# Performance work log

Measured on AMD Instinct MI355X. Metric: run time of the kernel, lower is better.

Reference implementation:

```python
import jax, jax.numpy as jnp
import numpy as np

B, T, CIN, H, W = 256, 19, 3, 24, 24
HID, LAST, K = 64, 128, 512
CC = 0.25  # commitment cost
NUM_DEC_LAYERS = 19


def setup_inputs() -> dict:
    key = jax.random.key(0)
    ks = jax.random.split(key, 19)
    def rn(k, shape, scale=0.05):
        return jax.random.normal(k, shape, jnp.float32) * scale
    return dict(
        x=jax.random.normal(ks[0], (B, T, CIN, H, W), jnp.float32),
        eps=jax.random.normal(ks[1], (B, LAST), jnp.float32),
        emb=jax.random.normal(ks[2], (K, HID), jnp.float32),
        enc_w0=rn(ks[3], (HID, CIN, 3, 3)), enc_w0_b=rn(ks[4], (HID,)),
        enc_w1=rn(ks[5], (2 * LAST, HID, 8, 8)), enc_w1_b=rn(ks[6], (2 * LAST,)),
        enc_r0=rn(ks[7], (HID, HID)), enc_r0_b=rn(ks[8], (HID,)),
        enc_lin_w=rn(ks[9], (2 * LAST, 2 * LAST)), enc_lin_b=rn(ks[10], (2 * LAST,)),
        dec_w0=rn(ks[11], (HID, CIN, 3, 3)), dec_w0_b=rn(ks[12], (CIN,)),
        dec_w1=rn(ks[13], (LAST, HID, 8, 8)), dec_w1_b=rn(ks[14], (HID,)),
        dec_r0=rn(ks[15], (HID, HID)), dec_r0_b=rn(ks[16], (HID,)),
        dec_lin_w=rn(ks[17], (LAST, LAST)), dec_lin_b=rn(ks[18], (LAST,)),
    )


def reference(x, eps, emb, enc_w0, enc_w0_b, enc_w1, enc_w1_b, enc_r0, enc_r0_b,
              enc_lin_w, enc_lin_b, dec_w0, dec_w0_b, dec_w1, dec_w1_b,
              dec_r0, dec_r0_b, dec_lin_w, dec_lin_b):
    relu = jax.nn.relu

    # ---- encoder (conv-RNN over time) ----
    def conv0(xt):  # Conv2d(CIN->HID, k=3, s=3): 24x24 -> 8x8
        y = jax.lax.conv_general_dilated(
            xt, enc_w0, (3, 3), 'VALID',
            dimension_numbers=('NCHW', 'OIHW', 'NCHW'))
        return y + enc_w0_b[None, :, None, None]

    def contract(h1):  # Conv2d(HID->2*LAST, k=8) on 8x8 == full contraction
        return jnp.einsum('bchw,ochw->bo', h1, enc_w1) + enc_w1_b

    h1 = relu(conv0(x[:, 0]))
    h2 = relu(contract(h1))

    def enc_step(carry, xt):
        h1, h2 = carry
        h1 = relu(conv0(xt) + jnp.einsum('bchw,oc->bohw', h1, enc_r0)
                  + enc_r0_b[None, :, None, None])
        h2h = relu(contract(h1))
        h2 = relu(h2h + h2 @ enc_lin_w.T + enc_lin_b)
        return (h1, h2), None

    (h1, h2), _ = jax.lax.scan(enc_step, (h1, h2), jnp.swapaxes(x[:, 1:], 0, 1))

    # ---- VQ (EMA codebook lookup; codebook carries no grad) ----
    zin = jnp.transpose(h1, (0, 2, 3, 1))        # [B, 8, 8, HID]
    flat = zin.reshape(-1, HID)                   # [B*64, HID]
    d = (jnp.sum(flat * flat, 1, keepdims=True)
         + jnp.sum(emb * emb, 1) - 2.0 * flat @ emb.T)
    idx = jnp.argmin(d, 1)                        # [B*64]
    q = emb[idx].reshape(zin.shape)
    loss_vq = CC * jnp.mean((jax.lax.stop_gradient(q) - zin) ** 2)
    q_st = zin + jax.lax.stop_gradient(q - zin)   # straight-through
    quantized = jnp.transpose(q_st, (0, 3, 1, 2)) # [B, HID, 8, 8]
    counts = jnp.zeros((K,), flat.dtype).at[idx].add(1.0)
    avg = counts / flat.shape[0]
    perplexity = jnp.exp(-jnp.sum(avg * jnp.log(avg + 1e-10)))

    # ---- KL(q(z|x) || N(0,1)) and reparam sample ----
    mu, logvar = jnp.split(h2, 2, axis=1)
    kl = jnp.mean(jnp.sum(0.5 * (jnp.exp(logvar) + mu * mu - 1.0 - logvar), axis=1))
    h2s = mu + jnp.exp(0.5 * logvar) * eps

    # ---- decoder (conv-RNN emitting 19 frames) ----
    def dec_update(h1c, h2c):
        h2c = relu(h2c @ dec_lin_w.T + dec_lin_b)
        h1h = jnp.einsum('bchw,oc->bohw', h1c, dec_r0) + dec_r0_b[None, :, None, None]
        h1l = jnp.einsum('bc,cohw->bohw', h2c, dec_w1) + dec_w1_b[None, :, None, None]
        return relu(h1h + h1l), h2c

    h1d, h2d = dec_update(quantized, h2s)  # i == 0: no emitted frame

    def dec_step(carry, _):
        h1c, h2c = carry
        h1c, h2c = dec_update(h1c, h2c)
        # ConvTranspose2d(HID->CIN, k=3, s=3): non-overlapping -> einsum + reshape
        y = jnp.einsum('bchw,coij->bohiwj', h1c, dec_w0).reshape(
            h1c.shape[0], CIN, 24, 24)
        layer = jax.nn.elu(y + dec_w0_b[None, :, None, None])
        return (h1c, h2c), layer

    _, layers = jax.lax.scan(dec_step, (h1d, h2d), None, length=NUM_DEC_LAYERS)
    x_tilde = jnp.swapaxes(layers, 0, 1)  # [B, 19, CIN, 24, 24]

    return (loss_vq, kl, x_tilde, perplexity)
```

## Files before the change

### kernel.cpp

```cpp
#include <hip/hip_runtime.h>
#include <math.h>

#define RL(x) __builtin_amdgcn_readfirstlane(x)

typedef short  s16x8 __attribute__((ext_vector_type(8)));
typedef float  f32x4 __attribute__((ext_vector_type(4)));

__device__ __forceinline__ float relu_(float v) { return v > 0.f ? v : 0.f; }
__device__ __forceinline__ unsigned short f2bf(float f) {
  unsigned u = __float_as_uint(f);
  u += 0x7FFFu + ((u >> 16) & 1u);
  return (unsigned short)(u >> 16);
}
__device__ __forceinline__ float bf2f(unsigned short h) {
  return __uint_as_float((unsigned)h << 16);
}

__global__ __launch_bounds__(256) void k_prep(
    const float* __restrict__ w1, const float* __restrict__ linw,
    const float* __restrict__ dlinw, const float* __restrict__ emb,
    const float* __restrict__ dw1,
    unsigned short* __restrict__ w1b, float* __restrict__ linT,
    float* __restrict__ dlinT, float* __restrict__ embsq,
    unsigned short* __restrict__ dw1b,
    float* __restrict__ scal, float* __restrict__ counts)
{
  int bid = blockIdx.x, tid = threadIdx.x;
  if (bid < 64) {
    #pragma unroll
    for (int j = 0; j < 32; ++j) {
      int idx = bid * 16384 + j * 512 + tid * 2;
      float2 v = *(const float2*)(w1 + idx);
      unsigned pk = ((unsigned)f2bf(v.y) << 16) | (unsigned)f2bf(v.x);
      *(unsigned*)&w1b[idx] = pk;
    }
    return;
  }
  if (bid == 84) {
    if (tid < 2) scal[tid] = 0.f;
    for (int j = tid; j < 512; j += 256) counts[j] = 0.f;
    return;
  }
  if (bid >= 85) {
    __shared__ float tbuf[64 * 65];
    int idx = bid - 85;
    int r0 = (idx >> 6) * 64, c0 = (idx & 63) * 64;
    int lane = tid & 63, grp = tid >> 6;
    for (int pp = 0; pp < 16; ++pp) {
      int rr = pp * 4 + grp;
      tbuf[rr * 65 + lane] = dw1[(size_t)(r0 + rr) * 4096 + c0 + lane];
    }
    __syncthreads();
    for (int pp = 0; pp < 16; ++pp) {
      int cc = pp * 4 + grp;
      dw1b[(size_t)(c0 + cc) * 128 + r0 + lane] = f2bf(tbuf[lane * 65 + cc]);
    }
    return;
  }
  if (bid >= 82) {
    int k = (bid - 82) * 256 + tid;
    const float* e = emb + k * 64;
    float s0 = 0, s1 = 0, s2 = 0, s3 = 0;
    #pragma unroll
    for (int c = 0; c < 64; c += 4) {
      s0 += e[c] * e[c]; s1 += e[c+1] * e[c+1];
      s2 += e[c+2] * e[c+2]; s3 += e[c+3] * e[c+3];
    }
    embsq[k] = (s0 + s1) + (s2 + s3);
    return;
  }
  __shared__ float buf[64 * 65];
  const float* in; float* out; int R, C, tr, tc;
  if (bid < 80) { in = linw;  out = linT;  R = 256; C = 256; tr = (bid - 64) >> 2; tc = (bid - 64) & 3; }
  else          { in = dlinw; out = dlinT; R = 128; C = 128; tr = (bid - 80) >> 1; tc = (bid - 80) & 1; }
  int r0 = tr * 64, c0 = tc * 64;
  int lane = tid & 63, grp = tid >> 6;
  for (int pp = 0; pp < 16; ++pp) {
    int rr = pp * 4 + grp;
    buf[rr * 65 + lane] = in[(r0 + rr) * C + c0 + lane];
  }
  __syncthreads();
  for (int pp = 0; pp < 16; ++pp) {
    int cc = pp * 4 + grp;
    out[(c0 + cc) * R + r0 + lane] = buf[lane * 65 + cc];
  }
}

__global__ __launch_bounds__(256) void k_conv0(
    const float* __restrict__ x, const float* __restrict__ w0,
    float* __restrict__ xconv)
{
  int bid = blockIdx.x, tid = threadIdx.x;
  int t = bid >> 8, b = bid & 255;
  int p = tid & 63, og = RL(tid >> 6);
  int i = p >> 3, j = p & 7;
  const float* xb = x + ((size_t)(b * 19 + t) * 3) * 576 + (i * 3) * 24 + j * 3;
  float xv[27];
  #pragma unroll
  for (int c = 0; c < 3; ++c)
    #pragma unroll
    for (int ki = 0; ki < 3; ++ki)
      #pragma unroll
      for (int kj = 0; kj < 3; ++kj)
        xv[c * 9 + ki * 3 + kj] = xb[c * 576 + ki * 24 + kj];
  float* op = xconv + ((size_t)(t * 256 + b) * 64 + og * 16) * 64 + p;
  #pragma unroll
  for (int q = 0; q < 16; ++q) {
    const float* wr = w0 + (og * 16 + q) * 27;
    float c0 = 0, c1 = 0, c2 = 0;
    #pragma unroll
    for (int m = 0; m < 27; m += 3) {
      c0 += xv[m] * wr[m]; c1 += xv[m+1] * wr[m+1]; c2 += xv[m+2] * wr[m+2];
    }
    op[q * 64] = (c0 + c1) + c2;
  }
}

__global__ __launch_bounds__(512) void k_encmma(
    const float* __restrict__ xconv,
    const float* __restrict__ w0b,
    const float* __restrict__ r0, const float* __restrict__ r0b,
    unsigned short* __restrict__ st_out,
    unsigned short* __restrict__ st_tail,
    float* __restrict__ h1f)
{
  __shared__ unsigned short Hs[2][4096];
  int b = blockIdx.x, tid = threadIdx.x;
  int l = tid & 63;
  int wv = RL(tid >> 6);
  int os = wv >> 1, ph = wv & 1;
  int co = os * 16 + (l >> 4) * 4;
  int arow = os * 16 + (l & 15);
  s16x8 avR[2];
  #pragma unroll
  for (int kk = 0; kk < 2; ++kk) {
    int cb = (kk * 4 + (l >> 4)) * 8;
    const float* src = r0 + arow * 64 + cb;
    #pragma unroll
    for (int j = 0; j < 8; ++j) avR[kk][j] = (short)f2bf(src[j]);
  }
  float b0v[4], b1v[4];
  #pragma unroll
  for (int r = 0; r < 4; ++r) {
    b0v[r] = w0b[co + r];
    b1v[r] = b0v[r] + r0b[co + r];
  }
  int pA = ph * 32 + (l & 15);
  int pB = pA + 16;

  float xcA[4], xcB[4];
  {
    const float* xc = xconv + ((size_t)b * 64 + co) * 64;
    #pragma unroll
    for (int r = 0; r < 4; ++r) {
      xcA[r] = xc[r * 64 + pA];
      xcB[r] = xc[r * 64 + pB];
    }
  }

  for (int t = 0; t <= 18; ++t) {
    f32x4 accA = (f32x4){0.f, 0.f, 0.f, 0.f};
    f32x4 accB = (f32x4){0.f, 0.f, 0.f, 0.f};
    if (t > 0) {
      const unsigned short* cbuf = Hs[(t & 1) ^ 1];
      #pragma unroll
      for (int kk = 0; kk < 2; ++kk) {
        int chk = kk * 4 + (l >> 4);
        s16x8 bvA = *(const s16x8*)&cbuf[pA * 64 + ((chk ^ (pA & 7)) << 3)];
        s16x8 bvB = *(const s16x8*)&cbuf[pB * 64 + ((chk ^ (pB & 7)) << 3)];
        accA = __builtin_amdgcn_mfma_f32_16x16x32_bf16(avR[kk], bvA, accA, 0, 0, 0);
        accB = __builtin_amdgcn_mfma_f32_16x16x32_bf16(avR[kk], bvB, accB, 0, 0, 0);
      }
    }
    unsigned short* so = (t < 16)
        ? st_out  + (size_t)t * 1048576 + (size_t)b * 4096
        : st_tail + (size_t)(t - 16) * 1048576 + (size_t)b * 4096;
    unsigned short* nb = Hs[t & 1];
    {
      float v0 = relu_(accA[0] + xcA[0] + (t ? b1v[0] : b0v[0]));
      float v1 = relu_(accA[1] + xcA[1] + (t ? b1v[1] : b0v[1]));
      float v2 = relu_(accA[2] + xcA[2] + (t ? b1v[2] : b0v[2]));
      float v3 = relu_(accA[3] + xcA[3] + (t ? b1v[3] : b0v[3]));
      uint2 pk;
      pk.x = (unsigned)f2bf(v0) | ((unsigned)f2bf(v1) << 16);
      pk.y = (unsigned)f2bf(v2) | ((unsigned)f2bf(v3) << 16);
      *(uint2*)&nb[pA * 64 + (((co >> 3) ^ (pA & 7)) << 3) + (co & 7)] = pk;
      so[(co + 0) * 64 + pA] = (unsigned short)(pk.x & 0xFFFF);
      so[(co + 1) * 64 + pA] = (unsigned short)(pk.x >> 16);
      so[(co + 2) * 64 + pA] = (unsigned short)(pk.y & 0xFFFF);
      so[(co + 3) * 64 + pA] = (unsigned short)(pk.y >> 16);
      if (t == 18) {
        h1f[(size_t)b * 4096 + (co + 0) * 64 + pA] = v0;
        h1f[(size_t)b * 4096 + (co + 1) * 64 + pA] = v1;
        h1f[(size_t)b * 4096 + (co + 2) * 64 + pA] = v2;
        h1f[(size_t)b * 4096 + (co + 3) * 64 + pA] = v3;
      }
    }
    {
      float v0 = relu_(accB[0] + xcB[0] + (t ? b1v[0] : b0v[0]));
      float v1 = relu_(accB[1] + xcB[1] + (t ? b1v[1] : b0v[1]));
      float v2 = relu_(accB[2] + xcB[2] + (t ? b1v[2] : b0v[2]));
      float v3 = relu_(accB[3] + xcB[3] + (t ? b1v[3] : b0v[3]));
      uint2 pk;
      pk.x = (unsigned)f2bf(v0) | ((unsigned)f2bf(v1) << 16);
      pk.y = (unsigned)f2bf(v2) | ((unsigned)f2bf(v3) << 16);
      *(uint2*)&nb[pB * 64 + (((co >> 3) ^ (pB & 7)) << 3) + (co & 7)] = pk;
      so[(co + 0) * 64 + pB] = (unsigned short)(pk.x & 0xFFFF);
      so[(co + 1) * 64 + pB] = (unsigned short)(pk.x >> 16);
      so[(co + 2) * 64 + pB] = (unsigned short)(pk.y & 0xFFFF);
      so[(co + 3) * 64 + pB] = (unsigned short)(pk.y >> 16);
      if (t == 18) {
        h1f[(size_t)b * 4096 + (co + 0) * 64 + pB] = v0;
        h1f[(size_t)b * 4096 + (co + 1) * 64 + pB] = v1;
        h1f[(size_t)b * 4096 + (co + 2) * 64 + pB] = v2;
        h1f[(size_t)b * 4096 + (co + 3) * 64 + pB] = v3;
      }
    }
    if (t < 18) {
      const float* xc = xconv + ((size_t)((t + 1) * 256 + b) * 64 + co) * 64;
      #pragma unroll
      for (int r = 0; r < 4; ++r) {
        xcA[r] = xc[r * 64 + pA];
        xcB[r] = xc[r * 64 + pB];
      }
    }
    __syncthreads();
  }
}

__global__ __launch_bounds__(1024) void k_encchain_fb(
    const float* __restrict__ x,
    const float* __restrict__ w0, const float* __restrict__ w0b,
    const float* __restrict__ r0, const float* __restrict__ r0b,
    unsigned short* __restrict__ st_out,
    unsigned short* __restrict__ st_tail,
    float* __restrict__ h1f)
{
  __shared__ float stA[4096];
  __shared__ float stB[4096];
  int b = blockIdx.x, tid = threadIdx.x;
  int p = tid & 63;
  int o0 = RL(tid >> 6) * 4;
  float* cur = stA;
  float* nxt = stB;

  for (int t = 0; t <= 18; ++t) {
    float acc[4];
    int i = p >> 3, j = p & 7;
    const float* xb = x + ((size_t)(b * 19 + t) * 3) * 576 + (i * 3) * 24 + j * 3;
    float xv[27];
    #pragma unroll
    for (int c = 0; c < 3; ++c)
      #pragma unroll
      for (int ki = 0; ki < 3; ++ki)
        #pragma unroll
        for (int kj = 0; kj < 3; ++kj)
          xv[c * 9 + ki * 3 + kj] = xb[c * 576 + ki * 24 + kj];
    #pragma unroll
    for (int q = 0; q < 4; ++q) {
      float a = w0b[o0 + q] + (t > 0 ? r0b[o0 + q] : 0.f);
      const float* wr = w0 + (o0 + q) * 27;
      float c0 = 0, c1 = 0, c2 = 0;
      #pragma unroll
      for (int m = 0; m < 27; m += 3) {
        c0 += xv[m] * wr[m]; c1 += xv[m+1] * wr[m+1]; c2 += xv[m+2] * wr[m+2];
      }
      acc[q] = a + c0 + c1 + c2;
    }
    if (t > 0) {
      for (int c = 0; c < 64; c += 4) {
        float h0 = cur[c * 64 + p],     h1v = cur[(c+1) * 64 + p];
        float h2v = cur[(c+2) * 64 + p], h3v = cur[(c+3) * 64 + p];
        #pragma unroll
        for (int q = 0; q < 4; ++q) {
          const float* rr = r0 + (o0 + q) * 64 + c;
          acc[q] += h0 * rr[0] + h1v * rr[1] + h2v * rr[2] + h3v * rr[3];
        }
      }
    }
    unsigned short* so = (t < 16)
        ? st_out  + (size_t)t * 1048576 + (size_t)b * 4096
        : st_tail + (size_t)(t - 16) * 1048576 + (size_t)b * 4096;
    #pragma unroll
    for (int q = 0; q < 4; ++q) {
      float v = relu_(acc[q]);
      nxt[(o0 + q) * 64 + p] = v;
      so[(o0 + q) * 64 + p] = f2bf(v);
      if (t == 18) h1f[(size_t)b * 4096 + (o0 + q) * 64 + p] = v;
    }
    __syncthreads();
    float* tmp = cur; cur = nxt; nxt = tmp;
  }
}

__global__ __launch_bounds__(256) void k_conmma4(
    const unsigned short* __restrict__ st_out,
    const unsigned short* __restrict__ st_tail,
    const unsigned short* __restrict__ w1b,
    float* __restrict__ partsk)
{
  __shared__ unsigned short As[32 * 64];
  __shared__ unsigned short Bs[128 * 64];
  int bid = blockIdx.x, tid = threadIdx.x;
  int kts = bid & 3;
  int rem0 = bid >> 2;
  int t = rem0 >> 4, rem = rem0 & 15;
  int mt = rem >> 1, nt = rem & 1;
  int b0 = mt * 32, n0 = nt * 128;
  const unsigned short* abase = ((t < 16)
      ? st_out  + (size_t)t * 1048576
      : st_tail + (size_t)(t - 16) * 1048576) + (size_t)b0 * 4096;
  int w = RL(tid >> 6), l = tid & 63;
  int rh = w >> 1, chf = w & 1;

  int ar = tid >> 3, ac = tid & 7;
  unsigned short* adst = &As[ar * 64 + ((ac ^ (ar & 7)) << 3)];
  const unsigned short* asrc = abase + (size_t)ar * 4096 + (ac << 3);

  f32x4 acc[4];
  #pragma unroll
  for (int u = 0; u < 4; ++u) acc[u] = (f32x4){0.f, 0.f, 0.f, 0.f};

  for (int kt = 0; kt < 16; ++kt) {
    int k0 = kts * 1024 + kt * 64;
    __syncthreads();
    *(s16x8*)adst = *(const s16x8*)(asrc + k0);
    #pragma unroll
    for (int cc = 0; cc < 4; ++cc) {
      int idx = cc * 256 + tid;
      int br = idx >> 3, bc = idx & 7;
      *(s16x8*)&Bs[br * 64 + ((bc ^ (br & 7)) << 3)] =
          *(const s16x8*)(w1b + (size_t)(n0 + br) * 4096 + k0 + (bc << 3));
    }
    __syncthreads();
    #pragma unroll
    for (int kk = 0; kk < 2; ++kk) {
      int arow = rh * 16 + (l & 15);
      int chk  = kk * 4 + (l >> 4);
      s16x8 av = *(const s16x8*)&As[arow * 64 + ((chk ^ (arow & 7)) << 3)];
      #pragma unroll
      for (int u = 0; u < 4; ++u) {
        int brow = (chf * 4 + u) * 16 + (l & 15);
        s16x8 bv = *(const s16x8*)&Bs[brow * 64 + ((chk ^ (brow & 7)) << 3)];
        acc[u] = __builtin_amdgcn_mfma_f32_16x16x32_bf16(av, bv, acc[u], 0, 0, 0);
      }
    }
  }
  float* pb = partsk + (size_t)kts * 1245184 + (size_t)t * 65536;
  int colbase = n0 + chf * 64 + (l & 15);
  int rowbase = b0 + rh * 16 + (l >> 4) * 4;
  #pragma unroll
  for (int u = 0; u < 4; ++u)
    #pragma unroll
    for (int r = 0; r < 4; ++r)
      pb[(size_t)(rowbase + r) * 256 + colbase + u * 16] = acc[u][r];
}

__global__ __launch_bounds__(256) void k_red4(
    const float* __restrict__ partsk, float* __restrict__ parts)
{
  size_t i = (size_t)blockIdx.x * 256 + threadIdx.x;
  parts[i] = (partsk[i] + partsk[1245184 + i])
           + (partsk[2 * 1245184 + i] + partsk[3 * 1245184 + i]);
}

__global__ __launch_bounds__(256) void k_conmma(
    const unsigned short* __restrict__ st_out,
    const unsigned short* __restrict__ st_tail,
    const unsigned short* __restrict__ w1b,
    float* __restrict__ parts)
{
  __shared__ unsigned short As[32 * 64];
  __shared__ unsigned short Bs[128 * 64];
  int bid = blockIdx.x, tid = threadIdx.x;
  int t = bid >> 4, rem = bid & 15;
  int mt = rem >> 1, nt = rem & 1;
  int b0 = mt * 32, n0 = nt * 128;
  const unsigned short* abase = ((t < 16)
      ? st_out  + (size_t)t * 1048576
      : st_tail + (size_t)(t - 16) * 1048576) + (size_t)b0 * 4096;
  int w = RL(tid >> 6), l = tid & 63;
  int rh = w >> 1, chf = w & 1;

  int ar = tid >> 3, ac = tid & 7;
  unsigned short* adst = &As[ar * 64 + ((ac ^ (ar & 7)) << 3)];
  const unsigned short* asrc = abase + (size_t)ar * 4096 + (ac << 3);

  f32x4 acc[4];
  #pragma unroll
  for (int u = 0; u < 4; ++u) acc[u] = (f32x4){0.f, 0.f, 0.f, 0.f};

  for (int kt = 0; kt < 64; ++kt) {
    int k0 = kt * 64;
    __syncthreads();
    *(s16x8*)adst = *(const s16x8*)(asrc + k0);
    #pragma unroll
    for (int cc = 0; cc < 4; ++cc) {
      int idx = cc * 256 + tid;
      int br = idx >> 3, bc = idx & 7;
      *(s16x8*)&Bs[br * 64 + ((bc ^ (br & 7)) << 3)] =
          *(const s16x8*)(w1b + (size_t)(n0 + br) * 4096 + k0 + (bc << 3));
    }
    __syncthreads();
    #pragma unroll
    for (int kk = 0; kk < 2; ++kk) {
      int arow = rh * 16 + (l & 15);
      int chk  = kk * 4 + (l >> 4);
      s16x8 av = *(const s16x8*)&As[arow * 64 + ((chk ^ (arow & 7)) << 3)];
      #pragma unroll
      for (int u = 0; u < 4; ++u) {
        int brow = (chf * 4 + u) * 16 + (l & 15);
        s16x8 bv = *(const s16x8*)&Bs[brow * 64 + ((chk ^ (brow & 7)) << 3)];
        acc[u] = __builtin_amdgcn_mfma_f32_16x16x32_bf16(av, bv, acc[u], 0, 0, 0);
      }
    }
  }
  float* pb = parts + (size_t)t * 65536;
  int colbase = n0 + chf * 64 + (l & 15);
  int rowbase = b0 + rh * 16 + (l >> 4) * 4;
  #pragma unroll
  for (int u = 0; u < 4; ++u)
    #pragma unroll
    for (int r = 0; r < 4; ++r)
      pb[(size_t)(rowbase + r) * 256 + colbase + u * 16] = acc[u][r];
}

__global__ __launch_bounds__(512, 1) void k_h2all(
    const float* __restrict__ parts, const float* __restrict__ w1b,
    const float* __restrict__ linT, const float* __restrict__ linb,
    const float* __restrict__ eps, float* __restrict__ scal,
    const float* __restrict__ dlinT, const float* __restrict__ dlinb,
    unsigned short* __restrict__ h2b)
{
  __shared__ float curL[256];
  __shared__ float ppart[512];
  __shared__ float red[256];
  int b = blockIdx.x, tid = threadIdx.x;
  int o  = tid & 255, kh = tid >> 8;
  float wreg[128];
  #pragma unroll
  for (int jj = 0; jj < 128; ++jj)
    wreg[jj] = linT[(kh * 128 + jj) * 256 + o];

  if (tid < 256)
    curL[tid] = relu_(parts[(size_t)b * 256 + tid] + w1b[tid]);
  __syncthreads();
  for (int t = 1; t <= 18; ++t) {
    float lacc = 0.f;
    #pragma unroll
    for (int jj = 0; jj < 128; ++jj)
      lacc += wreg[jj] * curL[kh * 128 + jj];
    ppart[tid] = lacc;
    __syncthreads();
    float v = 0.f;
    if (tid < 256) {
      float h2h = relu_(parts[(size_t)t * 65536 + (size_t)b * 256 + tid] + w1b[tid]);
      v = relu_(h2h + ppart[tid] + ppart[256 + tid] + linb[tid]);
    }
    __syncthreads();
    if (tid < 256) curL[tid] = v;
    __syncthreads();
  }
  if (tid < 128) {
    float mu = curL[tid], lv = curL[128 + tid];
    red[tid] = 0.5f * (expf(lv) + mu * mu - 1.0f - lv);
  }
  __syncthreads();
  for (int s = 64; s > 0; s >>= 1) {
    if (tid < s) red[tid] += red[tid + s];
    __syncthreads();
  }
  if (tid == 0) atomicAdd(&scal[1], red[0]);
  float hs = 0.f;
  if (tid < 128)
    hs = curL[tid] + expf(0.5f * curL[128 + tid]) * eps[(size_t)b * 128 + tid];
  __syncthreads();
  if (tid < 128) curL[tid] = hs;
  __syncthreads();

  int o2 = tid & 127, kh2 = (tid >> 7) & 1;
  float wreg2[64];
  if (tid < 256) {
    #pragma unroll
    for (int jj = 0; jj < 64; ++jj)
      wreg2[jj] = dlinT[(kh2 * 64 + jj) * 128 + o2];
  }
  for (int s = 0; s < 20; ++s) {
    float lacc = 0.f;
    if (tid < 256) {
      #pragma unroll
      for (int jj = 0; jj < 64; ++jj)
        lacc += wreg2[jj] * curL[kh2 * 64 + jj];
      ppart[tid] = lacc;
    }
    __syncthreads();
    float v = 0.f;
    if (tid < 128) {
      v = relu_(ppart[tid] + ppart[128 + tid] + dlinb[tid]);
      h2b[(size_t)s * 32768 + (size_t)b * 128 + tid] = f2bf(v);
    }
    __syncthreads();
    if (tid < 128) curL[tid] = v;
    __syncthreads();
  }
}

__global__ __launch_bounds__(256) void k_argmin(
    const float* __restrict__ h1f, const float* __restrict__ emb,
    const float* __restrict__ embsq,
    float* __restrict__ pbest, int* __restrict__ pidx)
{
  __shared__ float sd[256];
  __shared__ int   sk[256];
  int bid = blockIdx.x, tid = threadIdx.x;
  int qtr = bid >> 8, b = bid & 255;
  int p = tid & 63, kg = RL(tid >> 6);
  float f[64];
  const float* hb = h1f + (size_t)b * 4096 + p;
  #pragma unroll
  for (int c = 0; c < 64; ++c) f[c] = hb[c * 64];
  float best = 3.4e38f; int bk = 0;
  int kbeg = qtr * 128 + kg * 32;
  for (int k = kbeg; k < kbeg + 32; ++k) {
    const float* er = emb + k * 64;
    float d0 = 0, d1 = 0, d2 = 0, d3 = 0;
    #pragma unroll
    for (int c = 0; c < 64; c += 4) {
      d0 += f[c] * er[c];     d1 += f[c+1] * er[c+1];
      d2 += f[c+2] * er[c+2]; d3 += f[c+3] * er[c+3];
    }
    float d = embsq[k] - 2.f * ((d0 + d1) + (d2 + d3));
    if (d < best) { best = d; bk = k; }
  }
  sd[tid] = best; sk[tid] = bk;
  __syncthreads();
  if (tid < 64) {
    float bb = sd[tid]; int kk = sk[tid];
    #pragma unroll
    for (int g = 1; g < 4; ++g) {
      float dg = sd[g * 64 + tid];
      if (dg < bb) { bb = dg; kk = sk[g * 64 + tid]; }
    }
    pbest[qtr * 16384 + b * 64 + tid] = bb;
    pidx [qtr * 16384 + b * 64 + tid] = kk;
  }
}

__device__ __forceinline__ unsigned short* h1l_ptr(
    int d, int b, float* out, unsigned short* tail)
{
  if (d >= 1 && d <= 17)
    return (unsigned short*)(out + 2 + (size_t)b * 32832 + (size_t)(d - 1) * 1728);
  int slot = (d == 0) ? 0 : (d - 17);
  return tail + (size_t)slot * 1048576 + (size_t)b * 4096;
}

__global__ __launch_bounds__(256) void k_declmma(
    const unsigned short* __restrict__ h2b,
    const unsigned short* __restrict__ dw1b,
    float* __restrict__ out, unsigned short* __restrict__ tail)
{
  __shared__ unsigned short As[64 * 128];
  __shared__ unsigned short Bs[64 * 128];
  int bid = blockIdx.x, tid = threadIdx.x;
  int mt = bid >> 6, nt = bid & 63;
  int m0 = mt * 64, n0 = nt * 64;
  int w = RL(tid >> 6), l = tid & 63;

  #pragma unroll
  for (int cc = 0; cc < 4; ++cc) {
    int idx = cc * 256 + tid;
    int row = idx >> 4, col = idx & 15;
    *(s16x8*)&As[row * 128 + ((col ^ (row & 7)) << 3)] =
        *(const s16x8*)(h2b + (size_t)(m0 + row) * 128 + (col << 3));
    *(s16x8*)&Bs[row * 128 + ((col ^ (row & 7)) << 3)] =
        *(const s16x8*)(dw1b + (size_t)(n0 + row) * 128 + (col << 3));
  }
  __syncthreads();

  f32x4 acc[4];
  #pragma unroll
  for (int u = 0; u < 4; ++u) acc[u] = (f32x4){0.f, 0.f, 0.f, 0.f};
  int arow = w * 16 + (l & 15);
  #pragma unroll
  for (int kk = 0; kk < 4; ++kk) {
    int chk = kk * 4 + (l >> 4);
    s16x8 av = *(const s16x8*)&As[arow * 128 + ((chk ^ (arow & 7)) << 3)];
    #pragma unroll
    for (int u = 0; u < 4; ++u) {
      int brow = u * 16 + (l & 15);
      s16x8 bv = *(const s16x8*)&Bs[brow * 128 + ((chk ^ (brow & 7)) << 3)];
      acc[u] = __builtin_amdgcn_mfma_f32_16x16x32_bf16(av, bv, acc[u], 0, 0, 0);
    }
  }
  int d = m0 >> 8;
  #pragma unroll
  for (int r = 0; r < 4; ++r) {
    int b = (m0 & 255) + w * 16 + (l >> 4) * 4 + r;
    unsigned short* op = h1l_ptr(d, b, out, tail);
    #pragma unroll
    for (int u = 0; u < 4; ++u)
      op[n0 + u * 16 + (l & 15)] = f2bf(acc[u][r]);
  }
}

__global__ __launch_bounds__(256) void k_vqstats(
    const float* __restrict__ h1f, const float* __restrict__ emb,
    const float* __restrict__ pbest, const int* __restrict__ pidx,
    float* __restrict__ Q, float* __restrict__ counts,
    float* __restrict__ loss_sum)
{
  __shared__ int   fk[64];
  __shared__ int   lhist[512];
  __shared__ float red[256];
  int b = blockIdx.x, tid = threadIdx.x;
  for (int j = tid; j < 512; j += 256) lhist[j] = 0;
  __syncthreads();
  if (tid < 64) {
    float bb = pbest[b * 64 + tid];
    int   kk = pidx [b * 64 + tid];
    #pragma unroll
    for (int q = 1; q < 4; ++q) {
      float dq = pbest[q * 16384 + b * 64 + tid];
      if (dq < bb) { bb = dq; kk = pidx[q * 16384 + b * 64 + tid]; }
    }
    fk[tid] = kk;
    atomicAdd(&lhist[kk], 1);
  }
  __syncthreads();
  int p = tid & 63, cgi = tid >> 6;
  int kk = fk[p];
  const float* eb = emb + kk * 64 + cgi * 16;
  const float* hz = h1f + (size_t)b * 4096 + cgi * 1024 + p;
  float* qb = Q + (size_t)b * 4096 + cgi * 1024 + p;
  float ls = 0;
  #pragma unroll
  for (int c = 0; c < 16; ++c) {
    float e = eb[c];
    float z = hz[c * 64];
    float dd = e - z;
    ls += dd * dd;
    qb[c * 64] = e;
  }
  red[tid] = ls;
  __syncthreads();
  for (int s = 128; s > 0; s >>= 1) { if (tid < s) red[tid] += red[tid + s]; __syncthreads(); }
  if (tid == 0) atomicAdd(loss_sum, red[0]);
  for (int j = tid; j < 512; j += 256) {
    int h = lhist[j];
    if (h > 0) atomicAdd(&counts[j], (float)h);
  }
}

__global__ __launch_bounds__(1024) void k_decchain(
    const float* __restrict__ Q,
    const float* __restrict__ dr0, const float* __restrict__ dr0b,
    const float* __restrict__ dw1b_bias,
    const float* __restrict__ w0d, const float* __restrict__ w0db,
    float* __restrict__ out, unsigned short* __restrict__ tail,
    const float* __restrict__ counts, const float* __restrict__ scal)
{
  int bid = blockIdx.x, tid = threadIdx.x;
  if (bid == 256) {
    __shared__ float red[512];
    if (tid < 512) {
      float avg = counts[tid] * (1.0f / 16384.0f);
      red[tid] = avg * logf(avg + 1e-10f);
    }
    __syncthreads();
    for (int s = 256; s > 0; s >>= 1) {
      if (tid < s) red[tid] += red[tid + s];
      __syncthreads();
    }
    if (tid == 0) {
      out[0] = 0.25f * scal[0] * (1.0f / 1048576.0f);
      out[1] = scal[1] * (1.0f / 256.0f);
      out[2 + 8404992] = expf(-red[0]);
    }
    return;
  }
  __shared__ unsigned short Hs[2][4096];
  int b = bid;
  int l = tid & 63;
  int wv = RL(tid >> 6);

  for (int idx = tid; idx < 4096; idx += 1024) {
    int c = idx >> 6, p = idx & 63;
    Hs[0][p * 64 + ((((c >> 3) ^ (p & 7))) << 3) + (c & 7)] =
        f2bf(Q[(size_t)b * 4096 + idx]);
  }

  if (wv < 8) {
    int os = wv >> 1;
    int ph = wv & 1;
    int co = os * 16 + (l >> 4) * 4;
    int arow = os * 16 + (l & 15);
    s16x8 avR[2];
    #pragma unroll
    for (int kk = 0; kk < 2; ++kk) {
      int cb = (kk * 4 + (l >> 4)) * 8;
      const float* src = dr0 + arow * 64 + cb;
      #pragma unroll
      for (int j = 0; j < 8; ++j) avR[kk][j] = (short)f2bf(src[j]);
    }
    float biasv[4];
    #pragma unroll
    for (int r = 0; r < 4; ++r) biasv[r] = dr0b[co + r] + dw1b_bias[co + r];
    int pA = (ph * 2) * 16 + (l & 15);
    int pB = (ph * 2 + 1) * 16 + (l & 15);
    __syncthreads();

    for (int i = 0; i <= 20; ++i) {
      if (i <= 19) {
        const unsigned short* lp = h1l_ptr(i, b, out, tail);
        float hlA[4], hlB[4];
        #pragma unroll
        for (int r = 0; r < 4; ++r) {
          hlA[r] = bf2f(lp[(co + r) * 64 + pA]);
          hlB[r] = bf2f(lp[(co + r) * 64 + pB]);
        }
        const unsigned short* cb = Hs[i & 1];
        f32x4 accA = (f32x4){0.f, 0.f, 0.f, 0.f};
        f32x4 accB = (f32x4){0.f, 0.f, 0.f, 0.f};
        #pragma unroll
        for (int kk = 0; kk < 2; ++kk) {
          int chk = kk * 4 + (l >> 4);
          s16x8 bvA = *(const s16x8*)&cb[pA * 64 + ((chk ^ (pA & 7)) << 3)];
          s16x8 bvB = *(const s16x8*)&cb[pB * 64 + ((chk ^ (pB & 7)) << 3)];
          accA = __builtin_amdgcn_mfma_f32_16x16x32_bf16(avR[kk], bvA, accA, 0, 0, 0);
          accB = __builtin_amdgcn_mfma_f32_16x16x32_bf16(avR[kk], bvB, accB, 0, 0, 0);
        }
        unsigned short* nb = Hs[(i + 1) & 1];
        {
          float v0 = relu_(accA[0] + hlA[0] + biasv[0]);
          float v1 = relu_(accA[1] + hlA[1] + biasv[1]);
          float v2 = relu_(accA[2] + hlA[2] + biasv[2]);
          float v3 = relu_(accA[3] + hlA[3] + biasv[3]);
          uint2 pk;
          pk.x = (unsigned)f2bf(v0) | ((unsigned)f2bf(v1) << 16);
          pk.y = (unsigned)f2bf(v2) | ((unsigned)f2bf(v3) << 16);
          *(uint2*)&nb[pA * 64 + (((co >> 3) ^ (pA & 7)) << 3) + (co & 7)] = pk;
        }
        {
          float v0 = relu_(accB[0] + hlB[0] + biasv[0]);
          float v1 = relu_(accB[1] + hlB[1] + biasv[1]);
          float v2 = relu_(accB[2] + hlB[2] + biasv[2]);
          float v3 = relu_(accB[3] + hlB[3] + biasv[3]);
          uint2 pk;
          pk.x = (unsigned)f2bf(v0) | ((unsigned)f2bf(v1) << 16);
          pk.y = (unsigned)f2bf(v2) | ((unsigned)f2bf(v3) << 16);
          *(uint2*)&nb[pB * 64 + (((co >> 3) ^ (pB & 7)) << 3) + (co & 7)] = pk;
        }
      }
      __syncthreads();
    }
  } else {
    int job = wv - 8;
    int mt = job >> 2, pt = job & 3;
    int m0 = mt * 16 + (l >> 4) * 4;
    int am = mt * 16 + (l & 15);
    s16x8 avE[2];
    #pragma unroll
    for (int kk = 0; kk < 2; ++kk) {
      int cbg = (kk * 4 + (l >> 4)) * 8;
      #pragma unroll
      for (int j = 0; j < 8; ++j)
        avE[kk][j] = (am < 27) ? (short)f2bf(w0d[(cbg + j) * 27 + am]) : (short)0;
    }
    int p = pt * 16 + (l & 15);
    int hrow = p >> 3, wcol = p & 7;
    int preoff[4]; float eb[4]; bool vld[4];
    #pragma unroll
    for (int r = 0; r < 4; ++r) {
      int m = m0 + r;
      vld[r] = (m < 27);
      int mm = vld[r] ? m : 0;
      int o3 = mm / 9, rr = mm % 9, ki = rr / 3, kj = rr % 3;
      preoff[r] = o3 * 576 + (hrow * 3 + ki) * 24 + wcol * 3 + kj;
      eb[r] = w0db[o3];
    }
    __syncthreads();

    for (int i = 0; i <= 20; ++i) {
      if (i >= 2) {
        const unsigned short* cb = Hs[i & 1];
        f32x4 acc = (f32x4){0.f, 0.f, 0.f, 0.f};
        #pragma unroll
        for (int kk = 0; kk < 2; ++kk) {
          int chk = kk * 4 + (l >> 4);
          s16x8 bv = *(const s16x8*)&cb[p * 64 + ((chk ^ (p & 7)) << 3)];
          acc = __builtin_amdgcn_mfma_f32_16x16x32_bf16(avE[kk], bv, acc, 0, 0, 0);
        }
        int t = i - 2;
        float* fb = out + 2 + (size_t)(b * 19 + t) * 1728;
        #pragma unroll
        for (int r = 0; r < 4; ++r) {
          if (vld[r]) {
            float v = acc[r] + eb[r];
            v = v > 0.f ? v : expm1f(v);
            fb[preoff[r]] = v;
          }
        }
      }
      __syncthreads();
    }
  }
}

extern "C" void kernel_launch(void* const* d_in, const int* in_sizes, int n_in,
                              void* d_out, int out_size, void* d_ws, size_t ws_size,
                              hipStream_t stream)
{
  const float* x     = (const float*)d_in[0];
  const float* eps   = (const float*)d_in[1];
  const float* emb   = (const float*)d_in[2];
  const float* ew0   = (const float*)d_in[3];
  const float* ew0b  = (const float*)d_in[4];
  const float* ew1   = (const float*)d_in[5];
  const float* ew1b  = (const float*)d_in[6];
  const float* er0   = (const float*)d_in[7];
  const float* er0b  = (const float*)d_in[8];
  const float* elinw = (const float*)d_in[9];
  const float* elinb = (const float*)d_in[10];
  const float* dw0   = (const float*)d_in[11];
  const float* dw0b  = (const float*)d_in[12];
  const float* dw1   = (const float*)d_in[13];
  const float* dw1b  = (const float*)d_in[14];
  const float* dr0   = (const float*)d_in[15];
  const float* dr0b  = (const float*)d_in[16];
  const float* dlinw = (const float*)d_in[17];
  const float* dlinb = (const float*)d_in[18];
  float* out = (float*)d_out;
  float* ws  = (float*)d_ws;

  unsigned short* W1B = (unsigned short*)ws;
  float* Q      = ws + 0;
  float* LINT   = ws + 1048576;
  float* DLINT  = ws + 1114112;
  float* EMBSQ  = ws + 1130496;
  float* H1F    = ws + 1131008;
  float* PARTS  = ws + 2179584;
  float* PBEST  = ws + 2179584;
  int*   PIDX   = (int*)(ws + 2245120);
  unsigned short* TAIL = (unsigned short*)(ws + 3424768);
  unsigned short* H2B  = (unsigned short*)(ws + 4997632);
  unsigned short* DW1B = (unsigned short*)(ws + 5325312);
  float* SCAL   = ws + 5652992;
  float* COUNTS = ws + 5652994;
  const size_t XC_OFF = 5653508;
  const size_t XC_END = XC_OFF + (size_t)19 * 256 * 4096;
  bool big = ws_size >= XC_END * sizeof(float);
  float* XCONV = big ? (ws + XC_OFF) : nullptr;

  unsigned short* ST_OUT = (unsigned short*)(out + 2);

  k_prep<<<213, 256, 0, stream>>>(ew1, elinw, dlinw, emb, dw1, W1B, LINT,
                                  DLINT, EMBSQ, DW1B, SCAL, COUNTS);
  if (big) {
    k_conv0<<<4864, 256, 0, stream>>>(x, ew0, XCONV);
    k_encmma<<<256, 512, 0, stream>>>(XCONV, ew0b, er0, er0b,
                                      ST_OUT, TAIL, H1F);
    k_conmma4<<<1216, 256, 0, stream>>>(ST_OUT, TAIL, W1B, XCONV);
    k_red4<<<4864, 256, 0, stream>>>(XCONV, PARTS);
  } else {
    k_encchain_fb<<<256, 1024, 0, stream>>>(x, ew0, ew0b, er0, er0b,
                                            ST_OUT, TAIL, H1F);
    k_conmma<<<304, 256, 0, stream>>>(ST_OUT, TAIL, W1B, PARTS);
  }
  k_h2all<<<256, 512, 0, stream>>>(PARTS, ew1b, LINT, elinb, eps, SCAL,
                                   DLINT, dlinb, H2B);
  k_argmin<<<1024, 256, 0, stream>>>(H1F, emb, EMBSQ, PBEST, PIDX);
  k_declmma<<<5120, 256, 0, stream>>>(H2B, DW1B, out, TAIL);
  k_vqstats<<<256, 256, 0, stream>>>(H1F, emb, PBEST, PIDX, Q, COUNTS,
                                     &SCAL[0]);
  k_decchain<<<257, 1024, 0, stream>>>(Q, dr0, dr0b, dw1b, dw0, dw0b,
                                       out, TAIL, COUNTS, SCAL);
}
```

Measured before the change: 332.0 us.

## Fuse conv0 into encoder recurrence and fold split-K reduction into h2all

Computes the 3x3/stride-3 input convolution inside the recurrent encoder kernel, double-buffering each timestep's result in shared memory and prefetching the next frame's inputs, which removes the separate conv kernel and its large global intermediate. The contraction GEMM moves from 4 to 8 K-slices for more blocks. The separate reduction kernel is removed, and the h2 recurrence kernel now sums the slices inline. The trade-off is extra per-step conv work on the serial recurrence path and 8 strided global reads per element in h2all.

```diff
diff --git a/kernel.cpp b/kernel.cpp
--- a/kernel.cpp
+++ b/kernel.cpp
@@ -86,16 +86,8 @@
   }
 }
 
-__global__ __launch_bounds__(256) void k_conv0(
-    const float* __restrict__ x, const float* __restrict__ w0,
-    float* __restrict__ xconv)
-{
-  int bid = blockIdx.x, tid = threadIdx.x;
-  int t = bid >> 8, b = bid & 255;
-  int p = tid & 63, og = RL(tid >> 6);
-  int i = p >> 3, j = p & 7;
-  const float* xb = x + ((size_t)(b * 19 + t) * 3) * 576 + (i * 3) * 24 + j * 3;
-  float xv[27];
+__device__ __forceinline__ void loadx27(const float* __restrict__ xb,
+                                        float* xv) {
   #pragma unroll
   for (int c = 0; c < 3; ++c)
     #pragma unroll
@@ -103,28 +95,31 @@
       #pragma unroll
       for (int kj = 0; kj < 3; ++kj)
         xv[c * 9 + ki * 3 + kj] = xb[c * 576 + ki * 24 + kj];
-  float* op = xconv + ((size_t)(t * 256 + b) * 64 + og * 16) * 64 + p;
-  #pragma unroll
-  for (int q = 0; q < 16; ++q) {
-    const float* wr = w0 + (og * 16 + q) * 27;
+}
+__device__ __forceinline__ void prod8(const float* __restrict__ wb,
+                                      const float* xv, float* cvrow, int l) {
+  #pragma unroll
+  for (int q = 0; q < 8; ++q) {
+    const float* wr = wb + q * 27;
     float c0 = 0, c1 = 0, c2 = 0;
     #pragma unroll
     for (int m = 0; m < 27; m += 3) {
       c0 += xv[m] * wr[m]; c1 += xv[m+1] * wr[m+1]; c2 += xv[m+2] * wr[m+2];
     }
-    op[q * 64] = (c0 + c1) + c2;
+    cvrow[q * 64 + l] = (c0 + c1) + c2;
   }
 }
 
 __global__ __launch_bounds__(512) void k_encmma(
-    const float* __restrict__ xconv,
-    const float* __restrict__ w0b,
+    const float* __restrict__ x,
+    const float* __restrict__ w0, const float* __restrict__ w0b,
     const float* __restrict__ r0, const float* __restrict__ r0b,
     unsigned short* __restrict__ st_out,
     unsigned short* __restrict__ st_tail,
     float* __restrict__ h1f)
 {
   __shared__ unsigned short Hs[2][4096];
+  __shared__ float CV[2][4096];
   int b = blockIdx.x, tid = threadIdx.x;
   int l = tid & 63;
   int wv = RL(tid >> 6);
@@ -147,16 +142,17 @@
   }
   int pA = ph * 32 + (l & 15);
   int pB = pA + 16;
-
-  float xcA[4], xcB[4];
-  {
-    const float* xc = xconv + ((size_t)b * 64 + co) * 64;
-    #pragma unroll
-    for (int r = 0; r < 4; ++r) {
-      xcA[r] = xc[r * 64 + pA];
-      xcB[r] = xc[r * 64 + pB];
-    }
-  }
+  int ip = l >> 3, jp = l & 7;
+  const float* xbase = x + ((size_t)b * 19 * 3) * 576 + (ip * 3) * 24 + jp * 3;
+  const float* wb = w0 + wv * 8 * 27;
+  float* cvrow0 = &CV[0][wv * 8 * 64];
+  float* cvrow1 = &CV[1][wv * 8 * 64];
+
+  float xv[27];
+  loadx27(xbase, xv);
+  prod8(wb, xv, cvrow0, l);
+  loadx27(xbase + (size_t)3 * 576, xv);
+  __syncthreads();
 
   for (int t = 0; t <= 18; ++t) {
     f32x4 accA = (f32x4){0.f, 0.f, 0.f, 0.f};
@@ -172,15 +168,16 @@
         accB = __builtin_amdgcn_mfma_f32_16x16x32_bf16(avR[kk], bvB, accB, 0, 0, 0);
       }
     }
+    const float* cv = CV[t & 1];
     unsigned short* so = (t < 16)
         ? st_out  + (size_t)t * 1048576 + (size_t)b * 4096
         : st_tail + (size_t)(t - 16) * 1048576 + (size_t)b * 4096;
     unsigned short* nb = Hs[t & 1];
     {
-      float v0 = relu_(accA[0] + xcA[0] + (t ? b1v[0] : b0v[0]));
-      float v1 = relu_(accA[1] + xcA[1] + (t ? b1v[1] : b0v[1]));
-      float v2 = relu_(accA[2] + xcA[2] + (t ? b1v[2] : b0v[2]));
-      float v3 = relu_(accA[3] + xcA[3] + (t ? b1v[3] : b0v[3]));
+      float v0 = relu_(accA[0] + cv[(co + 0) * 64 + pA] + (t ? b1v[0] : b0v[0]));
+      float v1 = relu_(accA[1] + cv[(co + 1) * 64 + pA] + (t ? b1v[1] : b0v[1]));
+      float v2 = relu_(accA[2] + cv[(co + 2) * 64 + pA] + (t ? b1v[2] : b0v[2]));
+      float v3 = relu_(accA[3] + cv[(co + 3) * 64 + pA] + (t ? b1v[3] : b0v[3]));
       uint2 pk;
       pk.x = (unsigned)f2bf(v0) | ((unsigned)f2bf(v1) << 16);
       pk.y = (unsigned)f2bf(v2) | ((unsigned)f2bf(v3) << 16);
@@ -197,10 +194,10 @@
       }
     }
     {
-      float v0 = relu_(accB[0] + xcB[0] + (t ? b1v[0] : b0v[0]));
-      float v1 = relu_(accB[1] + xcB[1] + (t ? b1v[1] : b0v[1]));
-      float v2 = relu_(accB[2] + xcB[2] + (t ? b1v[2] : b0v[2]));
-      float v3 = relu_(accB[3] + xcB[3] + (t ? b1v[3] : b0v[3]));
+      float v0 = relu_(accB[0] + cv[(co + 0) * 64 + pB] + (t ? b1v[0] : b0v[0]));
+      float v1 = relu_(accB[1] + cv[(co + 1) * 64 + pB] + (t ? b1v[1] : b0v[1]));
+      float v2 = relu_(accB[2] + cv[(co + 2) * 64 + pB] + (t ? b1v[2] : b0v[2]));
+      float v3 = relu_(accB[3] + cv[(co + 3) * 64 + pB] + (t ? b1v[3] : b0v[3]));
       uint2 pk;
       pk.x = (unsigned)f2bf(v0) | ((unsigned)f2bf(v1) << 16);
       pk.y = (unsigned)f2bf(v2) | ((unsigned)f2bf(v3) << 16);
@@ -217,83 +214,15 @@
       }
     }
     if (t < 18) {
-      const float* xc = xconv + ((size_t)((t + 1) * 256 + b) * 64 + co) * 64;
-      #pragma unroll
-      for (int r = 0; r < 4; ++r) {
-        xcA[r] = xc[r * 64 + pA];
-        xcB[r] = xc[r * 64 + pB];
-      }
-    }
-    __syncthreads();
-  }
-}
-
-__global__ __launch_bounds__(1024) void k_encchain_fb(
-    const float* __restrict__ x,
-    const float* __restrict__ w0, const float* __restrict__ w0b,
-    const float* __restrict__ r0, const float* __restrict__ r0b,
-    unsigned short* __restrict__ st_out,
-    unsigned short* __restrict__ st_tail,
-    float* __restrict__ h1f)
-{
-  __shared__ float stA[4096];
-  __shared__ float stB[4096];
-  int b = blockIdx.x, tid = threadIdx.x;
-  int p = tid & 63;
-  int o0 = RL(tid >> 6) * 4;
-  float* cur = stA;
-  float* nxt = stB;
-
-  for (int t = 0; t <= 18; ++t) {
-    float acc[4];
-    int i = p >> 3, j = p & 7;
-    const float* xb = x + ((size_t)(b * 19 + t) * 3) * 576 + (i * 3) * 24 + j * 3;
-    float xv[27];
-    #pragma unroll
-    for (int c = 0; c < 3; ++c)
-      #pragma unroll
-      for (int ki = 0; ki < 3; ++ki)
-        #pragma unroll
-        for (int kj = 0; kj < 3; ++kj)
-          xv[c * 9 + ki * 3 + kj] = xb[c * 576 + ki * 24 + kj];
-    #pragma unroll
-    for (int q = 0; q < 4; ++q) {
-      float a = w0b[o0 + q] + (t > 0 ? r0b[o0 + q] : 0.f);
-      const float* wr = w0 + (o0 + q) * 27;
-      float c0 = 0, c1 = 0, c2 = 0;
-      #pragma unroll
-      for (int m = 0; m < 27; m += 3) {
-        c0 += xv[m] * wr[m]; c1 += xv[m+1] * wr[m+1]; c2 += xv[m+2] * wr[m+2];
-      }
-      acc[q] = a + c0 + c1 + c2;
-    }
-    if (t > 0) {
-      for (int c = 0; c < 64; c += 4) {
-        float h0 = cur[c * 64 + p],     h1v = cur[(c+1) * 64 + p];
-        float h2v = cur[(c+2) * 64 + p], h3v = cur[(c+3) * 64 + p];
-        #pragma unroll
-        for (int q = 0; q < 4; ++q) {
-          const float* rr = r0 + (o0 + q) * 64 + c;
-          acc[q] += h0 * rr[0] + h1v * rr[1] + h2v * rr[2] + h3v * rr[3];
-        }
-      }
-    }
-    unsigned short* so = (t < 16)
-        ? st_out  + (size_t)t * 1048576 + (size_t)b * 4096
-        : st_tail + (size_t)(t - 16) * 1048576 + (size_t)b * 4096;
-    #pragma unroll
-    for (int q = 0; q < 4; ++q) {
-      float v = relu_(acc[q]);
-      nxt[(o0 + q) * 64 + p] = v;
-      so[(o0 + q) * 64 + p] = f2bf(v);
-      if (t == 18) h1f[(size_t)b * 4096 + (o0 + q) * 64 + p] = v;
-    }
-    __syncthreads();
-    float* tmp = cur; cur = nxt; nxt = tmp;
-  }
-}
-
-__global__ __launch_bounds__(256) void k_conmma4(
+      prod8(wb, xv, (((t + 1) & 1) ? cvrow1 : cvrow0), l);
+      if (t < 17)
+        loadx27(xbase + (size_t)(t + 2) * 3 * 576, xv);
+    }
+    __syncthreads();
+  }
+}
+
+__global__ __launch_bounds__(256) void k_conmma8(
     const unsigned short* __restrict__ st_out,
     const unsigned short* __restrict__ st_tail,
     const unsigned short* __restrict__ w1b,
@@ -302,8 +231,8 @@
   __shared__ unsigned short As[32 * 64];
   __shared__ unsigned short Bs[128 * 64];
   int bid = blockIdx.x, tid = threadIdx.x;
-  int kts = bid & 3;
-  int rem0 = bid >> 2;
+  int kts = bid & 7;
+  int rem0 = bid >> 3;
   int t = rem0 >> 4, rem = rem0 & 15;
   int mt = rem >> 1, nt = rem & 1;
   int b0 = mt * 32, n0 = nt * 128;
@@ -321,8 +250,8 @@
   #pragma unroll
   for (int u = 0; u < 4; ++u) acc[u] = (f32x4){0.f, 0.f, 0.f, 0.f};
 
-  for (int kt = 0; kt < 16; ++kt) {
-    int k0 = kts * 1024 + kt * 64;
+  for (int kt = 0; kt < 8; ++kt) {
+    int k0 = kts * 512 + kt * 64;
     __syncthreads();
     *(s16x8*)adst = *(const s16x8*)(asrc + k0);
     #pragma unroll
@@ -335,9 +264,9 @@
     __syncthreads();
     #pragma unroll
     for (int kk = 0; kk < 2; ++kk) {
-      int arow = rh * 16 + (l & 15);
-      int chk  = kk * 4 + (l >> 4);
-      s16x8 av = *(const s16x8*)&As[arow * 64 + ((chk ^ (arow & 7)) << 3)];
+      int arw = rh * 16 + (l & 15);
+      int chk = kk * 4 + (l >> 4);
+      s16x8 av = *(const s16x8*)&As[arw * 64 + ((chk ^ (arw & 7)) << 3)];
       #pragma unroll
       for (int u = 0; u < 4; ++u) {
         int brow = (chf * 4 + u) * 16 + (l & 15);
@@ -354,14 +283,6 @@
     #pragma unroll
     for (int r = 0; r < 4; ++r)
       pb[(size_t)(rowbase + r) * 256 + colbase + u * 16] = acc[u][r];
-}
-
-__global__ __launch_bounds__(256) void k_red4(
-    const float* __restrict__ partsk, float* __restrict__ parts)
-{
-  size_t i = (size_t)blockIdx.x * 256 + threadIdx.x;
-  parts[i] = (partsk[i] + partsk[1245184 + i])
-           + (partsk[2 * 1245184 + i] + partsk[3 * 1245184 + i]);
 }
 
 __global__ __launch_bounds__(256) void k_conmma(
@@ -404,9 +325,9 @@
     __syncthreads();
     #pragma unroll
     for (int kk = 0; kk < 2; ++kk) {
-      int arow = rh * 16 + (l & 15);
-      int chk  = kk * 4 + (l >> 4);
-      s16x8 av = *(const s16x8*)&As[arow * 64 + ((chk ^ (arow & 7)) << 3)];
+      int arw = rh * 16 + (l & 15);
+      int chk = kk * 4 + (l >> 4);
+      s16x8 av = *(const s16x8*)&As[arw * 64 + ((chk ^ (arw & 7)) << 3)];
       #pragma unroll
       for (int u = 0; u < 4; ++u) {
         int brow = (chf * 4 + u) * 16 + (l & 15);
@@ -425,8 +346,16 @@
       pb[(size_t)(rowbase + r) * 256 + colbase + u * 16] = acc[u][r];
 }
 
+__device__ __forceinline__ float psum(const float* __restrict__ p,
+                                      size_t off, int n) {
+  float s = p[off];
+  for (int u = 1; u < n; ++u) s += p[(size_t)u * 1245184 + off];
+  return s;
+}
+
 __global__ __launch_bounds__(512, 1) void k_h2all(
-    const float* __restrict__ parts, const float* __restrict__ w1b,
+    const float* __restrict__ partsk, int nslc,
+    const float* __restrict__ w1b,
     const float* __restrict__ linT, const float* __restrict__ linb,
     const float* __restrict__ eps, float* __restrict__ scal,
     const float* __restrict__ dlinT, const float* __restrict__ dlinb,
@@ -443,7 +372,7 @@
     wreg[jj] = linT[(kh * 128 + jj) * 256 + o];
 
   if (tid < 256)
-    curL[tid] = relu_(parts[(size_t)b * 256 + tid] + w1b[tid]);
+    curL[tid] = relu_(psum(partsk, (size_t)b * 256 + tid, nslc) + w1b[tid]);
   __syncthreads();
   for (int t = 1; t <= 18; ++t) {
     float lacc = 0.f;
@@ -454,7 +383,8 @@
     __syncthreads();
     float v = 0.f;
     if (tid < 256) {
-      float h2h = relu_(parts[(size_t)t * 65536 + (size_t)b * 256 + tid] + w1b[tid]);
+      float h2h = relu_(psum(partsk, (size_t)t * 65536 + (size_t)b * 256 + tid,
+                             nslc) + w1b[tid]);
       v = relu_(h2h + ppart[tid] + ppart[256 + tid] + linb[tid]);
     }
     __syncthreads();
@@ -848,27 +778,27 @@
   float* SCAL   = ws + 5652992;
   float* COUNTS = ws + 5652994;
   const size_t XC_OFF = 5653508;
-  const size_t XC_END = XC_OFF + (size_t)19 * 256 * 4096;
+  const size_t XC_END = XC_OFF + (size_t)8 * 1245184;
   bool big = ws_size >= XC_END * sizeof(float);
-  float* XCONV = big ? (ws + XC_OFF) : nullptr;
+  float* PARTSK = big ? (ws + XC_OFF) : nullptr;
 
   unsigned short* ST_OUT = (unsigned short*)(out + 2);
 
   k_prep<<<213, 256, 0, stream>>>(ew1, elinw, dlinw, emb, dw1, W1B, LINT,
                                   DLINT, EMBSQ, DW1B, SCAL, COUNTS);
+  k_encmma<<<256, 512, 0, stream>>>(x, ew0, ew0b, er0, er0b,
+                                    ST_OUT, TAIL, H1F);
+  const float* parts_src;
+  int nslc;
   if (big) {
-    k_conv0<<<4864, 256, 0, stream>>>(x, ew0, XCONV);
-    k_encmma<<<256, 512, 0, stream>>>(XCONV, ew0b, er0, er0b,
-                                      ST_OUT, TAIL, H1F);
-    k_conmma4<<<1216, 256, 0, stream>>>(ST_OUT, TAIL, W1B, XCONV);
-    k_red4<<<4864, 256, 0, stream>>>(XCONV, PARTS);
+    k_conmma8<<<2432, 256, 0, stream>>>(ST_OUT, TAIL, W1B, PARTSK);
+    parts_src = PARTSK; nslc = 8;
   } else {
-    k_encchain_fb<<<256, 1024, 0, stream>>>(x, ew0, ew0b, er0, er0b,
-                                            ST_OUT, TAIL, H1F);
     k_conmma<<<304, 256, 0, stream>>>(ST_OUT, TAIL, W1B, PARTS);
-  }
-  k_h2all<<<256, 512, 0, stream>>>(PARTS, ew1b, LINT, elinb, eps, SCAL,
-                                   DLINT, dlinb, H2B);
+    parts_src = PARTS; nslc = 1;
+  }
+  k_h2all<<<256, 512, 0, stream>>>(parts_src, nslc, ew1b, LINT, elinb, eps,
+                                   SCAL, DLINT, dlinb, H2B);
   k_argmin<<<1024, 256, 0, stream>>>(H1F, emb, EMBSQ, PBEST, PIDX);
   k_declmma<<<5120, 256, 0, stream>>>(H2B, DW1B, out, TAIL);
   k_vqstats<<<256, 256, 0, stream>>>(H1F, emb, PBEST, PIDX, Q, COUNTS,
```

Result: slower. 342.7 us (+3.2%).
